# Kernel optimization log

Hardware: AMD Instinct MI355X
Metric: run time of the kernel (lower is better)

Reference implementation:

```python
import jax, jax.numpy as jnp
import numpy as np
from jax import lax

VOCAB = 32000
D_MODEL = 1024
N_LAYERS = 4
D_STATE = 8
D_CONV = 4
EXPAND = 2
D_INNER = EXPAND * D_MODEL          # 2048
DT_RANK = (D_MODEL + 15) // 16      # 64
B, L = 2, 1024


def setup_inputs() -> dict:
    key = jax.random.key(0)
    ks = jax.random.split(key, 20)
    s = 0.02
    inp = {
        "input_ids": jax.random.randint(ks[0], (B, L), 0, VOCAB, dtype=jnp.int32),
        "embed": jax.random.normal(ks[1], (VOCAB, D_MODEL), jnp.float32) * s,
        "in_proj_w": jax.random.normal(ks[2], (N_LAYERS, 2 * D_INNER, D_MODEL), jnp.float32) * s,
        "conv_w": jax.random.normal(ks[3], (N_LAYERS, D_INNER, 1, D_CONV), jnp.float32) * s,
        "conv_b": jnp.zeros((N_LAYERS, D_INNER), jnp.float32),
        "x_proj_w": jax.random.normal(ks[4], (N_LAYERS, DT_RANK + 2 * D_STATE, D_INNER), jnp.float32) * s,
        "dt_proj_w": jax.random.normal(ks[5], (N_LAYERS, D_INNER, DT_RANK), jnp.float32) * s,
        "dt_proj_b": jax.random.normal(ks[6], (N_LAYERS, D_INNER), jnp.float32) * 0.1,
        "A_log": jnp.broadcast_to(jnp.log(jnp.arange(1, D_STATE + 1, dtype=jnp.float32)),
                                  (N_LAYERS, D_INNER, D_STATE)) + 0.0,
        "D": jnp.ones((N_LAYERS, D_INNER), jnp.float32),
        "out_proj_w": jax.random.normal(ks[7], (N_LAYERS, D_MODEL, D_INNER), jnp.float32) * s,
        "ln_g": jnp.ones((N_LAYERS, D_MODEL), jnp.float32),
        "ln_b": jnp.zeros((N_LAYERS, D_MODEL), jnp.float32),
        "fn_g": jnp.ones((D_MODEL,), jnp.float32),
        "fn_b": jnp.zeros((D_MODEL,), jnp.float32),
        "fc_w": jax.random.normal(ks[8], (VOCAB, D_MODEL), jnp.float32) * s,
        "fc_b": jnp.zeros((VOCAB,), jnp.float32),
    }
    return inp


def layer_norm(x, g, b, eps=1e-5):
    mu = jnp.mean(x, -1, keepdims=True)
    var = jnp.var(x, -1, keepdims=True)
    return (x - mu) * lax.rsqrt(var + eps) * g + b


def silu(x):
    return x * jax.nn.sigmoid(x)


def selective_scan(deltaA, deltaBu, C):
    # deltaA, deltaBu: (b,l,d,n); C: (b,l,n) -> y: (b,l,d)
    def step(h, inp):
        dA, dBu, c = inp
        h = dA * h + dBu                       # (b,d,n)
        y = jnp.einsum('bdn,bn->bd', h, c)
        return h, y
    h0 = jnp.zeros(deltaA.shape[:1] + deltaA.shape[2:], deltaA.dtype)
    _, ys = lax.scan(step, h0, (deltaA.transpose(1, 0, 2, 3),
                                deltaBu.transpose(1, 0, 2, 3),
                                C.transpose(1, 0, 2)))
    return ys.transpose(1, 0, 2)


def mamba_block(x, in_proj_w, conv_w, conv_b, x_proj_w, dt_proj_w, dt_proj_b, A_log, D, out_proj_w):
    # x: (b,l,d_model)
    xz = jnp.einsum('bld,ed->ble', x, in_proj_w)          # (b,l,2*di)
    xc, z = jnp.split(xz, 2, axis=-1)
    # causal depthwise conv1d, kernel D_CONV
    xc_ncl = xc.transpose(0, 2, 1)                         # (b,di,l)
    xc_ncl = lax.conv_general_dilated(
        xc_ncl, conv_w, window_strides=(1,), padding=[(D_CONV - 1, 0)],
        feature_group_count=D_INNER, dimension_numbers=('NCH', 'OIH', 'NCH'))
    xc = silu(xc_ncl.transpose(0, 2, 1) + conv_b)          # (b,l,di)
    x_dbl = jnp.einsum('bld,ed->ble', xc, x_proj_w)        # (b,l,dt_rank+2n)
    dt, Bm, Cm = jnp.split(x_dbl, [DT_RANK, DT_RANK + D_STATE], axis=-1)
    dt = jax.nn.softplus(jnp.einsum('blr,dr->bld', dt, dt_proj_w) + dt_proj_b)  # (b,l,di)
    A = -jnp.exp(A_log)                                    # (di,n)
    deltaA = jnp.exp(dt[..., None] * A)                    # (b,l,di,n)
    deltaBu = dt[..., None] * Bm[:, :, None, :] * xc[..., None]
    y = selective_scan(deltaA, deltaBu, Cm)                # (b,l,di)
    y = y + xc * D
    y = y * silu(z)
    return jnp.einsum('ble,de->bld', y, out_proj_w)


def reference(input_ids, embed, in_proj_w, conv_w, conv_b, x_proj_w, dt_proj_w,
              dt_proj_b, A_log, D, out_proj_w, ln_g, ln_b, fn_g, fn_b, fc_w, fc_b):
    x = embed[input_ids]                                   # (b,l,d)
    for i in range(N_LAYERS):
        out = mamba_block(x, in_proj_w[i], conv_w[i], conv_b[i], x_proj_w[i],
                          dt_proj_w[i], dt_proj_b[i], A_log[i], D[i], out_proj_w[i])
        x = layer_norm(out + x, ln_g[i], ln_b[i])
    x = layer_norm(x, fn_g, fn_b)
    logits = jnp.einsum('bld,vd->blv', x, fc_w) + fc_b
    return logits
```

## Files before the change

kernel.cpp:

```cpp
#include <hip/hip_runtime.h>
#include <cstddef>
#include <cstdint>

#define D_MODEL 1024
#define D_INNER 2048
#define DT_RANK 64
#define D_STATE 8
#define NLAYERS 4
#define BATCH 2
#define SEQ 1024
#define M_ROWS (BATCH*SEQ)
#define VOCAB 32000
#define XPAD 128
#define NC 32
#define LC 32
#define XSK 8

typedef __attribute__((ext_vector_type(8))) short short8;
typedef __attribute__((ext_vector_type(4))) float f32x4;

#define GPTR(p) (const __attribute__((address_space(1))) void*)(p)
#define LPTR(p) (__attribute__((address_space(3))) void*)(p)

__device__ __forceinline__ float sigmoidf_(float x) { return 1.f / (1.f + __expf(-x)); }

__device__ __forceinline__ unsigned short f2bf(float f) {
    unsigned u = __float_as_uint(f);
    u += 0x7fffu + ((u >> 16) & 1u);
    return (unsigned short)(u >> 16);
}
__device__ __forceinline__ float bf2f(unsigned short u) {
    return __uint_as_float((unsigned)u << 16);
}

__global__ __launch_bounds__(256) void cast_kernel(const float* __restrict__ in,
                                                   unsigned short* __restrict__ out, int n4)
{
    int i = blockIdx.x * 256 + threadIdx.x;
    if (i >= n4) return;
    float4 v = ((const float4*)in)[i];
    ushort4 o;
    o.x = f2bf(v.x); o.y = f2bf(v.y); o.z = f2bf(v.z); o.w = f2bf(v.w);
    ((ushort4*)out)[i] = o;
}

__global__ __launch_bounds__(256) void cast_pad_xproj(const float* __restrict__ in,
                                                      unsigned short* __restrict__ out)
{
    int i = blockIdx.x * 256 + threadIdx.x;
    if (i >= NLAYERS * XPAD * D_INNER / 4) return;
    int col4 = i & (D_INNER / 4 - 1);
    int row = (i >> 9) & (XPAD - 1);
    int layer = i >> 16;
    ushort4 o = {0, 0, 0, 0};
    if (row < 80) {
        float4 v = ((const float4*)(in + ((size_t)layer * 80 + row) * D_INNER))[col4];
        o.x = f2bf(v.x); o.y = f2bf(v.y); o.z = f2bf(v.z); o.w = f2bf(v.w);
    }
    ((ushort4*)out)[i] = o;
}

__global__ __launch_bounds__(256) void gather_kernel(const int* __restrict__ ids,
                                                     const float* __restrict__ embed,
                                                     float* __restrict__ x,
                                                     unsigned short* __restrict__ xb)
{
    int m = blockIdx.x;
    int t = threadIdx.x;
    int id = ids[m];
    float4 v = ((const float4*)(embed + (size_t)id * D_MODEL))[t];
    ((float4*)(x + (size_t)m * D_MODEL))[t] = v;
    ushort4 o;
    o.x = f2bf(v.x); o.y = f2bf(v.y); o.z = f2bf(v.z); o.w = f2bf(v.w);
    ((ushort4*)(xb + (size_t)m * D_MODEL))[t] = o;
}

template<int EPI>
__global__ __launch_bounds__(256) void gemm_bf16_nt(const unsigned short* __restrict__ A, int lda,
                                                    const unsigned short* __restrict__ B, int ldb,
                                                    void* __restrict__ Cv, int ldc,
                                                    int K, const float* __restrict__ bias)
{
    __shared__ unsigned short As[2][128 * 32];
    __shared__ unsigned short Bs[2][128 * 32];
    const int tid = threadIdx.x;

    const int gm = gridDim.x;
    const int bid = blockIdx.y * gm + blockIdx.x;
    const int q = (gm * gridDim.y) >> 3;
    const int swz = (bid & 7) * q + (bid >> 3);
    const int bm = (swz % gm) * 128, bn = (swz / gm) * 128;

    const int wid = tid >> 6, lane = tid & 63;
    const int wm = (wid >> 1) * 64, wn = (wid & 1) * 64;
    const int lrow = lane & 15, lkg = lane >> 4;

    const int srow = tid >> 2;
    const int ksrc = ((tid & 3) ^ ((srow >> 1) & 3)) * 8;
    const size_t kz = (size_t)blockIdx.z * K;
    const unsigned short* Ag = A + (size_t)(bm + srow) * lda + kz + ksrc;
    const unsigned short* Bg = B + (size_t)(bn + srow) * ldb + kz + ksrc;
    const size_t r64a = (size_t)64 * lda;
    const size_t r64b = (size_t)64 * ldb;

#define STAGE(buf, koff)                                                                              \
    do {                                                                                              \
        __builtin_amdgcn_global_load_lds(GPTR(Ag + (koff)),        LPTR(&As[buf][tid * 8]), 16, 0, 0);\
        __builtin_amdgcn_global_load_lds(GPTR(Ag + r64a + (koff)), LPTR(&As[buf][2048 + tid * 8]), 16, 0, 0);\
        __builtin_amdgcn_global_load_lds(GPTR(Bg + (koff)),        LPTR(&Bs[buf][tid * 8]), 16, 0, 0);\
        __builtin_amdgcn_global_load_lds(GPTR(Bg + r64b + (koff)), LPTR(&Bs[buf][2048 + tid * 8]), 16, 0, 0);\
    } while (0)

    f32x4 acc[4][4];
    #pragma unroll
    for (int i = 0; i < 4; ++i)
        #pragma unroll
        for (int j = 0; j < 4; ++j)
            acc[i][j] = f32x4{0.f, 0.f, 0.f, 0.f};

    STAGE(0, 0);

    int cur = 0;
    for (int k0 = 0; k0 < K; k0 += 32) {
        if (k0 + 32 < K) {
            STAGE(cur ^ 1, k0 + 32);
            asm volatile("s_waitcnt vmcnt(4)" ::: "memory");
        } else {
            asm volatile("s_waitcnt vmcnt(0)" ::: "memory");
        }
        __builtin_amdgcn_s_barrier();
        __builtin_amdgcn_sched_barrier(0);

        short8 af[4], bf[4];
        #pragma unroll
        for (int i = 0; i < 4; ++i) {
            int ra = wm + 16 * i + lrow;
            int pa = lkg ^ ((ra >> 1) & 3);
            af[i] = *(const short8*)(&As[cur][ra * 32 + pa * 8]);
            int rb = wn + 16 * i + lrow;
            int pb = lkg ^ ((rb >> 1) & 3);
            bf[i] = *(const short8*)(&Bs[cur][rb * 32 + pb * 8]);
        }
        __builtin_amdgcn_s_setprio(1);
        #pragma unroll
        for (int i = 0; i < 4; ++i)
            #pragma unroll
            for (int j = 0; j < 4; ++j)
                acc[i][j] = __builtin_amdgcn_mfma_f32_16x16x32_bf16(af[i], bf[j], acc[i][j], 0, 0, 0);
        __builtin_amdgcn_s_setprio(0);

        __builtin_amdgcn_s_barrier();
        cur ^= 1;
    }
#undef STAGE

    const int crow = bm + wm + lkg * 4;
    const int ccol = bn + wn + lrow;
    #pragma unroll
    for (int i = 0; i < 4; ++i) {
        #pragma unroll
        for (int j = 0; j < 4; ++j) {
            float bv = (EPI == 2 || EPI == 3) ? bias[ccol + 16 * j] : 0.f;
            #pragma unroll
            for (int r = 0; r < 4; ++r) {
                float v = acc[i][j][r] + bv;
                size_t off = (size_t)(crow + 16 * i + r) * ldc + ccol + 16 * j;
                if (EPI == 0) {
                    ((float*)Cv)[(size_t)blockIdx.z * M_ROWS * ldc + off] = v;
                } else if (EPI == 2) {
                    ((float*)Cv)[off] = v;
                } else {
                    if (EPI == 3) v = (v > 20.f) ? v : log1pf(__expf(v));
                    ((unsigned short*)Cv)[off] = f2bf(v);
                }
            }
        }
    }
}

__device__ __forceinline__ void rd_a8(const unsigned short* S, int base, int lrow, int lkg, short8 a[4][2]) {
    #pragma unroll
    for (int i = 0; i < 4; ++i)
        #pragma unroll
        for (int kk = 0; kk < 2; ++kk) {
            int row = base + i * 16 + lrow;
            int p = (kk * 4 + lkg) ^ (lrow & 7);
            a[i][kk] = *(const short8*)(S + row * 64 + p * 8);
        }
}
__device__ __forceinline__ void rd_b4(const unsigned short* S, int base, int lrow, int lkg, short8 b[2][2]) {
    #pragma unroll
    for (int j = 0; j < 2; ++j)
        #pragma unroll
        for (int kk = 0; kk < 2; ++kk) {
            int row = base + j * 16 + lrow;
            int p = (kk * 4 + lkg) ^ (lrow & 7);
            b[j][kk] = *(const short8*)(S + row * 64 + p * 8);
        }
}

__global__ __launch_bounds__(512) void gemm_bf16_8ph(const unsigned short* __restrict__ A, int lda,
                                                     const unsigned short* __restrict__ B, int ldb,
                                                     float* __restrict__ C, int ldc,
                                                     int K, const float* __restrict__ bias)
{
    __shared__ unsigned short As[2][256 * 64];
    __shared__ unsigned short Bs[2][256 * 64];
    const int tid = threadIdx.x;

    const int gm = gridDim.x;
    const int bid = blockIdx.y * gm + blockIdx.x;
    const int q = (gm * gridDim.y) >> 3;
    const int swz = (bid & 7) * q + (bid >> 3);
    const int bm = (swz % gm) * 256, bn = (swz / gm) * 256;

    const int wid = tid >> 6, lane = tid & 63;
    const int wr = wid >> 2, wc = wid & 3;
    const int arow0 = wr * 128, brow0 = wc * 64;
    const int lrow = lane & 15, lkg = lane >> 4;

    const int sg = tid >> 3, su = tid & 7;
    const int ksrc = (su ^ (sg & 7)) * 8;
    const unsigned short* Ag = A + (size_t)(bm + sg) * lda + ksrc;
    const unsigned short* Bg = B + (size_t)(bn + sg) * ldb + ksrc;

#define STG_A(buf, kt) do {                                                                                        \
    __builtin_amdgcn_global_load_lds(GPTR(Ag + (size_t)(kt) * 64),                       LPTR(&As[buf][tid * 8]), 16, 0, 0); \
    __builtin_amdgcn_global_load_lds(GPTR(Ag + (size_t)(kt) * 64 + (size_t)64 * lda),    LPTR(&As[buf][4096 + tid * 8]), 16, 0, 0); \
    __builtin_amdgcn_global_load_lds(GPTR(Ag + (size_t)(kt) * 64 + (size_t)128 * lda),   LPTR(&As[buf][8192 + tid * 8]), 16, 0, 0); \
    __builtin_amdgcn_global_load_lds(GPTR(Ag + (size_t)(kt) * 64 + (size_t)192 * lda),   LPTR(&As[buf][12288 + tid * 8]), 16, 0, 0); \
} while (0)
#define STG_B(buf, kt) do {                                                                                        \
    __builtin_amdgcn_global_load_lds(GPTR(Bg + (size_t)(kt) * 64),                       LPTR(&Bs[buf][tid * 8]), 16, 0, 0); \
    __builtin_amdgcn_global_load_lds(GPTR(Bg + (size_t)(kt) * 64 + (size_t)64 * ldb),    LPTR(&Bs[buf][4096 + tid * 8]), 16, 0, 0); \
    __builtin_amdgcn_global_load_lds(GPTR(Bg + (size_t)(kt) * 64 + (size_t)128 * ldb),   LPTR(&Bs[buf][8192 + tid * 8]), 16, 0, 0); \
    __builtin_amdgcn_global_load_lds(GPTR(Bg + (size_t)(kt) * 64 + (size_t)192 * ldb),   LPTR(&Bs[buf][12288 + tid * 8]), 16, 0, 0); \
} while (0)
#define MFMA_Q(IH, JH) do {                                                                                        \
    __builtin_amdgcn_s_setprio(1);                                                                                 \
    _Pragma("unroll") for (int i = 0; i < 4; ++i)                                                                  \
    _Pragma("unroll") for (int j = 0; j < 2; ++j)                                                                  \
    _Pragma("unroll") for (int kk = 0; kk < 2; ++kk)                                                               \
        acc[(IH) * 4 + i][(JH) * 2 + j] =                                                                          \
            __builtin_amdgcn_mfma_f32_16x16x32_bf16(a[i][kk], b[j][kk], acc[(IH) * 4 + i][(JH) * 2 + j], 0, 0, 0); \
    __builtin_amdgcn_s_setprio(0);                                                                                 \
} while (0)
#define PBAR() __builtin_amdgcn_s_barrier()

    f32x4 acc[8][4];
    #pragma unroll
    for (int i = 0; i < 8; ++i)
        #pragma unroll
        for (int j = 0; j < 4; ++j)
            acc[i][j] = f32x4{0.f, 0.f, 0.f, 0.f};

    short8 a[4][2], b[2][2];
    const int NT = K >> 6;

    STG_A(0, 0); STG_B(0, 0); STG_A(1, 1);
    asm volatile("s_waitcnt vmcnt(4)" ::: "memory");
    PBAR();

    int buf = 0;
    for (int U = 0; U < NT; ++U, buf ^= 1) {
        if (U + 1 < NT) STG_B(buf ^ 1, U + 1);
        rd_a8(As[buf], arow0, lrow, lkg, a);
        rd_b4(Bs[buf], brow0, lrow, lkg, b);
        PBAR(); __builtin_amdgcn_sched_barrier(0);
        MFMA_Q(0, 0);
        PBAR();
        rd_b4(Bs[buf], brow0 + 32, lrow, lkg, b);
        PBAR(); __builtin_amdgcn_sched_barrier(0);
        MFMA_Q(0, 1);
        PBAR();
        rd_a8(As[buf], arow0 + 64, lrow, lkg, a);
        PBAR(); __builtin_amdgcn_sched_barrier(0);
        MFMA_Q(1, 1);
        PBAR();
        rd_b4(Bs[buf], brow0, lrow, lkg, b);
        if (U + 2 < NT) {
            STG_A(buf, U + 2);
            asm volatile("s_waitcnt vmcnt(4)" ::: "memory");
        } else {
            asm volatile("s_waitcnt vmcnt(0)" ::: "memory");
        }
        PBAR(); __builtin_amdgcn_sched_barrier(0);
        MFMA_Q(1, 0);
        PBAR();
    }
#undef STG_A
#undef STG_B
#undef MFMA_Q
#undef PBAR

    const int crow = bm + arow0 + lkg * 4;
    const int ccol = bn + brow0 + lrow;
    #pragma unroll
    for (int i = 0; i < 8; ++i) {
        #pragma unroll
        for (int j = 0; j < 4; ++j) {
            float bv = bias[ccol + 16 * j];
            float* Cp = C + (size_t)(crow + 16 * i) * ldc + ccol + 16 * j;
            #pragma unroll
            for (int r = 0; r < 4; ++r)
                Cp[(size_t)r * ldc] = acc[i][j][r] + bv;
        }
    }
}

__global__ __launch_bounds__(256) void reduce_xdbl(const float* __restrict__ part,
                                                   float* __restrict__ xdbl,
                                                   unsigned short* __restrict__ xdbl_b)
{
    int i = blockIdx.x * 256 + threadIdx.x;
    float4 s = ((const float4*)part)[i];
    #pragma unroll
    for (int z = 1; z < XSK; ++z) {
        float4 v = ((const float4*)part)[(size_t)z * (M_ROWS * XPAD / 4) + i];
        s.x += v.x; s.y += v.y; s.z += v.z; s.w += v.w;
    }
    ((float4*)xdbl)[i] = s;
    ushort4 o;
    o.x = f2bf(s.x); o.y = f2bf(s.y); o.z = f2bf(s.z); o.w = f2bf(s.w);
    ((ushort4*)xdbl_b)[i] = o;
}

__global__ __launch_bounds__(256) void conv_silu_kernel(const unsigned short* __restrict__ xzb,
                                                        const float* __restrict__ cw,
                                                        const float* __restrict__ cb,
                                                        unsigned short* __restrict__ xcb)
{
    int idx = blockIdx.x * 256 + threadIdx.x;
    int d = idx & (D_INNER - 1);
    int m = idx >> 11;
    int l = m & (SEQ - 1);
    int b = m >> 10;
    float w0 = cw[d * 4 + 0], w1 = cw[d * 4 + 1], w2 = cw[d * 4 + 2], w3 = cw[d * 4 + 3];
    float s = cb[d];
    const unsigned short* base = xzb + ((size_t)b * SEQ) * (2 * D_INNER) + d;
    if (l - 3 >= 0) s += bf2f(base[(size_t)(l - 3) * (2 * D_INNER)]) * w0;
    if (l - 2 >= 0) s += bf2f(base[(size_t)(l - 2) * (2 * D_INNER)]) * w1;
    if (l - 1 >= 0) s += bf2f(base[(size_t)(l - 1) * (2 * D_INNER)]) * w2;
    s += bf2f(base[(size_t)l * (2 * D_INNER)]) * w3;
    float v = s * sigmoidf_(s);
    xcb[(size_t)m * D_INNER + d] = f2bf(v);
}

__global__ __launch_bounds__(256) void scan_partial(const unsigned short* __restrict__ dtb,
                                                    const float* __restrict__ xdbl,
                                                    const unsigned short* __restrict__ xcb,
                                                    const float* __restrict__ A_log,
                                                    float* __restrict__ H,
                                                    float* __restrict__ P)
{
    const int tid = threadIdx.x;
    const int b = blockIdx.x & 1;
    const int c = (blockIdx.x >> 1) & (NC - 1);
    const int d = ((blockIdx.x >> 6) << 8) + tid;

    __shared__ float Bsm[LC][8];
    {
        int r = tid >> 3, n = tid & 7;
        Bsm[r][n] = xdbl[(size_t)(b * SEQ + c * LC + r) * XPAD + DT_RANK + n];
    }
    __syncthreads();

    float An[8];
    #pragma unroll
    for (int n = 0; n < 8; ++n) An[n] = -__expf(A_log[d * 8 + n]);
    float h[8] = {0.f,0.f,0.f,0.f,0.f,0.f,0.f,0.f};
    float p[8] = {1.f,1.f,1.f,1.f,1.f,1.f,1.f,1.f};

    const unsigned short* dtp = dtb + (size_t)(b * SEQ + c * LC) * D_INNER + d;
    const unsigned short* xcp = xcb + (size_t)(b * SEQ + c * LC) * D_INNER + d;
    for (int l = 0; l < LC; ++l) {
        float dtv = bf2f(dtp[(size_t)l * D_INNER]);
        float ux  = dtv * bf2f(xcp[(size_t)l * D_INNER]);
        #pragma unroll
        for (int n = 0; n < 8; ++n) {
            float dA = __expf(dtv * An[n]);
            h[n] = dA * h[n] + Bsm[l][n] * ux;
            p[n] *= dA;
        }
    }
    size_t base = (size_t)((b * NC + c) * 8) * D_INNER + d;
    #pragma unroll
    for (int n = 0; n < 8; ++n) {
        H[base + (size_t)n * D_INNER] = h[n];
        P[base + (size_t)n * D_INNER] = p[n];
    }
}

__global__ __launch_bounds__(256) void scan_combine(const float* __restrict__ H,
                                                    float* __restrict__ P )
{
    int idx = blockIdx.x * 256 + threadIdx.x;
    int d = idx & (D_INNER - 1);
    int n = (idx >> 11) & 7;
    int b = idx >> 14;
    float hp = 0.f;
    for (int c = 0; c < NC; ++c) {
        size_t base = (size_t)((b * NC + c) * 8 + n) * D_INNER + d;
        float Pv = P[base], Hv = H[base];
        P[base] = hp;
        hp = Pv * hp + Hv;
    }
}

__global__ __launch_bounds__(256) void scan_final(const unsigned short* __restrict__ dtb,
                                                  const float* __restrict__ xdbl,
                                                  const unsigned short* __restrict__ xcb,
                                                  const unsigned short* __restrict__ xzb,
                                                  const float* __restrict__ A_log,
                                                  const float* __restrict__ Dp,
                                                  const float* __restrict__ h0,
                                                  unsigned short* __restrict__ yb)
{
    const int tid = threadIdx.x;
    const int b = blockIdx.x & 1;
    const int c = (blockIdx.x >> 1) & (NC - 1);
    const int d = ((blockIdx.x >> 6) << 8) + tid;

    __shared__ float Bsm[LC][8];
    __shared__ float Csm[LC][8];
    {
        int r = tid >> 3, n = tid & 7;
        size_t xrow = (size_t)(b * SEQ + c * LC + r) * XPAD;
        Bsm[r][n] = xdbl[xrow + DT_RANK + n];
        Csm[r][n] = xdbl[xrow + DT_RANK + 8 + n];
    }
    __syncthreads();

    float An[8], h[8];
    size_t base = (size_t)((b * NC + c) * 8) * D_INNER + d;
    #pragma unroll
    for (int n = 0; n < 8; ++n) {
        An[n] = -__expf(A_log[d * 8 + n]);
        h[n] = h0[base + (size_t)n * D_INNER];
    }
    const float Dv = Dp[d];

    const unsigned short* dtp = dtb + (size_t)(b * SEQ + c * LC) * D_INNER + d;
    const unsigned short* xcp = xcb + (size_t)(b * SEQ + c * LC) * D_INNER + d;
    const unsigned short* zp  = xzb + (size_t)(b * SEQ + c * LC) * (2 * D_INNER) + D_INNER + d;
    unsigned short* ybp = yb + (size_t)(b * SEQ + c * LC) * D_INNER + d;

    for (int l = 0; l < LC; ++l) {
        float dtv = bf2f(dtp[(size_t)l * D_INNER]);
        float xcv = bf2f(xcp[(size_t)l * D_INNER]);
        float zv  = bf2f(zp[(size_t)l * (2 * D_INNER)]);
        float ux = dtv * xcv;
        float acc = 0.f;
        #pragma unroll
        for (int n = 0; n < 8; ++n) {
            float dA = __expf(dtv * An[n]);
            h[n] = dA * h[n] + Bsm[l][n] * ux;
            acc += h[n] * Csm[l][n];
        }
        float yv = (acc + xcv * Dv) * (zv * sigmoidf_(zv));
        ybp[(size_t)l * D_INNER] = f2bf(yv);
    }
}

template<bool ADD>
__global__ __launch_bounds__(256) void ln_kernel(const float* __restrict__ extra,
                                                 const float* __restrict__ xin,
                                                 float* __restrict__ xout,
                                                 unsigned short* __restrict__ xbout,
                                                 const float* __restrict__ g,
                                                 const float* __restrict__ bb)
{
    int m = blockIdx.x;
    int t = threadIdx.x;
    float4 v = ((const float4*)(xin + (size_t)m * D_MODEL))[t];
    if (ADD) {
        float4 e = ((const float4*)(extra + (size_t)m * D_MODEL))[t];
        v.x += e.x; v.y += e.y; v.z += e.z; v.w += e.w;
    }
    float s  = v.x + v.y + v.z + v.w;
    float s2 = v.x * v.x + v.y * v.y + v.z * v.z + v.w * v.w;
    for (int off = 32; off; off >>= 1) {
        s  += __shfl_down(s, off);
        s2 += __shfl_down(s2, off);
    }
    __shared__ float red[8];
    int wid = t >> 6, lane = t & 63;
    if (lane == 0) { red[wid] = s; red[wid + 4] = s2; }
    __syncthreads();
    if (t == 0) {
        float a  = red[0] + red[1] + red[2] + red[3];
        float b2 = red[4] + red[5] + red[6] + red[7];
        float mu = a * (1.f / D_MODEL);
        red[0] = mu;
        red[4] = b2 * (1.f / D_MODEL) - mu * mu;
    }
    __syncthreads();
    float mu = red[0];
    float rs = rsqrtf(red[4] + 1e-5f);
    float4 gg = ((const float4*)g)[t];
    float4 bv = ((const float4*)bb)[t];
    float4 o;
    o.x = (v.x - mu) * rs * gg.x + bv.x;
    o.y = (v.y - mu) * rs * gg.y + bv.y;
    o.z = (v.z - mu) * rs * gg.z + bv.z;
    o.w = (v.w - mu) * rs * gg.w + bv.w;
    ((float4*)(xout + (size_t)m * D_MODEL))[t] = o;
    ushort4 ob;
    ob.x = f2bf(o.x); ob.y = f2bf(o.y); ob.z = f2bf(o.z); ob.w = f2bf(o.w);
    ((ushort4*)(xbout + (size_t)m * D_MODEL))[t] = ob;
}

extern "C" void kernel_launch(void* const* d_in, const int* in_sizes, int n_in,
                              void* d_out, int out_size, void* d_ws, size_t ws_size,
                              hipStream_t stream)
{
    const int*   ids      = (const int*)d_in[0];
    const float* embed    = (const float*)d_in[1];
    const float* in_proj  = (const float*)d_in[2];
    const float* conv_w   = (const float*)d_in[3];
    const float* conv_b   = (const float*)d_in[4];
    const float* x_proj   = (const float*)d_in[5];
    const float* dt_w     = (const float*)d_in[6];
    const float* dt_b     = (const float*)d_in[7];
    const float* A_log    = (const float*)d_in[8];
    const float* Dp       = (const float*)d_in[9];
    const float* out_proj = (const float*)d_in[10];
    const float* ln_g     = (const float*)d_in[11];
    const float* ln_b     = (const float*)d_in[12];
    const float* fn_g     = (const float*)d_in[13];
    const float* fn_b     = (const float*)d_in[14];
    const float* fc_w     = (const float*)d_in[15];
    const float* fc_b     = (const float*)d_in[16];
    float* logits = (float*)d_out;

    float* ws = (float*)d_ws;
    float* x     = ws;
    float* xdbl  = x + (size_t)M_ROWS * D_MODEL;
    float* tmp   = xdbl + (size_t)M_ROWS * XPAD;
    float* xpart = tmp + (size_t)M_ROWS * D_MODEL;

    float* Hbuf = tmp;
    float* Pbuf = tmp + (size_t)BATCH * NC * D_STATE * D_INNER;

    unsigned short* xb     = (unsigned short*)(xpart + (size_t)XSK * M_ROWS * XPAD);
    unsigned short* yb     = xb + (size_t)M_ROWS * D_MODEL;
    unsigned short* xzb    = yb + (size_t)M_ROWS * D_INNER;
    unsigned short* xcb    = xzb + (size_t)M_ROWS * 2 * D_INNER;
    unsigned short* dtb    = xcb + (size_t)M_ROWS * D_INNER;
    unsigned short* xdbl_b = dtb + (size_t)M_ROWS * D_INNER;
    unsigned short* wb_in  = xdbl_b + (size_t)M_ROWS * XPAD;
    unsigned short* wb_out = wb_in + (size_t)NLAYERS * 2 * D_INNER * D_MODEL;
    unsigned short* wb_fc  = wb_out + (size_t)NLAYERS * D_MODEL * D_INNER;
    unsigned short* wb_x   = wb_fc + (size_t)VOCAB * D_MODEL;
    unsigned short* wb_dt  = wb_x + (size_t)NLAYERS * XPAD * D_INNER;

    {
        int n4 = NLAYERS * 2 * D_INNER * D_MODEL / 4;
        cast_kernel<<<(n4 + 255) / 256, 256, 0, stream>>>(in_proj, wb_in, n4);
        n4 = NLAYERS * D_MODEL * D_INNER / 4;
        cast_kernel<<<(n4 + 255) / 256, 256, 0, stream>>>(out_proj, wb_out, n4);
        n4 = VOCAB * D_MODEL / 4;
        cast_kernel<<<(n4 + 255) / 256, 256, 0, stream>>>(fc_w, wb_fc, n4);
        n4 = NLAYERS * D_INNER * DT_RANK / 4;
        cast_kernel<<<(n4 + 255) / 256, 256, 0, stream>>>(dt_w, wb_dt, n4);
        n4 = NLAYERS * XPAD * D_INNER / 4;
        cast_pad_xproj<<<(n4 + 255) / 256, 256, 0, stream>>>(x_proj, wb_x);
    }

    gather_kernel<<<M_ROWS, 256, 0, stream>>>(ids, embed, x, xb);

    for (int i = 0; i < NLAYERS; ++i) {
        const unsigned short* W_in_b  = wb_in + (size_t)i * 2 * D_INNER * D_MODEL;
        const unsigned short* W_out_b = wb_out + (size_t)i * D_MODEL * D_INNER;
        const unsigned short* W_x_b   = wb_x + (size_t)i * XPAD * D_INNER;
        const unsigned short* W_dt_b  = wb_dt + (size_t)i * D_INNER * DT_RANK;
        const float* cw    = conv_w + (size_t)i * D_INNER * 4;
        const float* cb    = conv_b + (size_t)i * D_INNER;
        const float* b_dt  = dt_b + (size_t)i * D_INNER;
        const float* Al    = A_log + (size_t)i * D_INNER * D_STATE;
        const float* Dl    = Dp + (size_t)i * D_INNER;
        const float* g     = ln_g + (size_t)i * D_MODEL;
        const float* bb    = ln_b + (size_t)i * D_MODEL;

        gemm_bf16_nt<1><<<dim3(M_ROWS / 128, 2 * D_INNER / 128), 256, 0, stream>>>(
            xb, D_MODEL, W_in_b, D_MODEL, xzb, 2 * D_INNER, D_MODEL, nullptr);

        conv_silu_kernel<<<(M_ROWS * D_INNER) / 256, 256, 0, stream>>>(xzb, cw, cb, xcb);

        gemm_bf16_nt<0><<<dim3(M_ROWS / 128, 1, XSK), 256, 0, stream>>>(
            xcb, D_INNER, W_x_b, D_INNER, xpart, XPAD, D_INNER / XSK, nullptr);
        reduce_xdbl<<<(M_ROWS * XPAD / 4) / 256, 256, 0, stream>>>(xpart, xdbl, xdbl_b);

        gemm_bf16_nt<3><<<dim3(M_ROWS / 128, D_INNER / 128), 256, 0, stream>>>(
            xdbl_b, XPAD, W_dt_b, DT_RANK, dtb, D_INNER, DT_RANK, b_dt);

        scan_partial<<<BATCH * NC * (D_INNER / 256), 256, 0, stream>>>(
            dtb, xdbl, xcb, Al, Hbuf, Pbuf);
        scan_combine<<<(BATCH * D_STATE * D_INNER) / 256, 256, 0, stream>>>(Hbuf, Pbuf);
        scan_final<<<BATCH * NC * (D_INNER / 256), 256, 0, stream>>>(
            dtb, xdbl, xcb, xzb, Al, Dl, Pbuf, yb);

        gemm_bf16_nt<0><<<dim3(M_ROWS / 128, D_MODEL / 128), 256, 0, stream>>>(
            yb, D_INNER, W_out_b, D_INNER, tmp, D_MODEL, D_INNER, nullptr);

        ln_kernel<true><<<M_ROWS, 256, 0, stream>>>(tmp, x, x, xb, g, bb);
    }

    ln_kernel<false><<<M_ROWS, 256, 0, stream>>>(nullptr, x, tmp, xb, fn_g, fn_b);

    gemm_bf16_8ph<<<dim3(M_ROWS / 256, VOCAB / 256), 512, 0, stream>>>(
        xb, D_MODEL, wb_fc, D_MODEL, logits, VOCAB, D_MODEL, fc_b);
}
```

Baseline: 1.002 ms.

## Split-K out_proj and x_proj, and pipeline LM-head GEMM loads per half-tile

The LM-head 8-phase GEMM now stages A and B in half-tile chunks spread across the phases of a two-tile unrolled loop. Each warp also takes two separated 32-column B slices instead of one contiguous 64-column slice. This is meant to smooth memory traffic against MFMA work and shorten exposed load waits. Separately, out_proj becomes split-K by 2, with the partial sums added inside the residual LayerNorm, and x_proj split-K goes from 8 to 16 to raise parallelism in small GEMMs. The cost is more partial-buffer traffic and more complex wait counting.

```diff
diff --git a/kernel.cpp b/kernel.cpp
--- a/kernel.cpp
+++ b/kernel.cpp
@@ -14,7 +14,8 @@
 #define XPAD 128
 #define NC 32
 #define LC 32
-#define XSK 8
+#define XSK 16
+#define OSK 2
 
 typedef __attribute__((ext_vector_type(8))) short short8;
 typedef __attribute__((ext_vector_type(4))) float f32x4;
@@ -216,7 +217,8 @@
 
     const int wid = tid >> 6, lane = tid & 63;
     const int wr = wid >> 2, wc = wid & 3;
-    const int arow0 = wr * 128, brow0 = wc * 64;
+    const int arow0 = wr * 128;
+    const int b0r = wc * 32, b1r = 128 + wc * 32;
     const int lrow = lane & 15, lkg = lane >> 4;
 
     const int sg = tid >> 3, su = tid & 7;
@@ -224,28 +226,32 @@
     const unsigned short* Ag = A + (size_t)(bm + sg) * lda + ksrc;
     const unsigned short* Bg = B + (size_t)(bn + sg) * ldb + ksrc;
 
-#define STG_A(buf, kt) do {                                                                                        \
-    __builtin_amdgcn_global_load_lds(GPTR(Ag + (size_t)(kt) * 64),                       LPTR(&As[buf][tid * 8]), 16, 0, 0); \
-    __builtin_amdgcn_global_load_lds(GPTR(Ag + (size_t)(kt) * 64 + (size_t)64 * lda),    LPTR(&As[buf][4096 + tid * 8]), 16, 0, 0); \
-    __builtin_amdgcn_global_load_lds(GPTR(Ag + (size_t)(kt) * 64 + (size_t)128 * lda),   LPTR(&As[buf][8192 + tid * 8]), 16, 0, 0); \
-    __builtin_amdgcn_global_load_lds(GPTR(Ag + (size_t)(kt) * 64 + (size_t)192 * lda),   LPTR(&As[buf][12288 + tid * 8]), 16, 0, 0); \
+#define STG_A_H(buf, kt, h) do {                                                                   \
+    __builtin_amdgcn_global_load_lds(GPTR(Ag + (size_t)(kt) * 64 + (size_t)((h) * 128) * lda),     \
+                                     LPTR(&As[buf][(h) * 8192 + tid * 8]), 16, 0, 0);              \
+    __builtin_amdgcn_global_load_lds(GPTR(Ag + (size_t)(kt) * 64 + (size_t)((h) * 128 + 64) * lda),\
+                                     LPTR(&As[buf][(h) * 8192 + 4096 + tid * 8]), 16, 0, 0);       \
 } while (0)
-#define STG_B(buf, kt) do {                                                                                        \
-    __builtin_amdgcn_global_load_lds(GPTR(Bg + (size_t)(kt) * 64),                       LPTR(&Bs[buf][tid * 8]), 16, 0, 0); \
-    __builtin_amdgcn_global_load_lds(GPTR(Bg + (size_t)(kt) * 64 + (size_t)64 * ldb),    LPTR(&Bs[buf][4096 + tid * 8]), 16, 0, 0); \
-    __builtin_amdgcn_global_load_lds(GPTR(Bg + (size_t)(kt) * 64 + (size_t)128 * ldb),   LPTR(&Bs[buf][8192 + tid * 8]), 16, 0, 0); \
-    __builtin_amdgcn_global_load_lds(GPTR(Bg + (size_t)(kt) * 64 + (size_t)192 * ldb),   LPTR(&Bs[buf][12288 + tid * 8]), 16, 0, 0); \
+#define STG_B_H(buf, kt, h) do {                                                                   \
+    __builtin_amdgcn_global_load_lds(GPTR(Bg + (size_t)(kt) * 64 + (size_t)((h) * 128) * ldb),     \
+                                     LPTR(&Bs[buf][(h) * 8192 + tid * 8]), 16, 0, 0);              \
+    __builtin_amdgcn_global_load_lds(GPTR(Bg + (size_t)(kt) * 64 + (size_t)((h) * 128 + 64) * ldb),\
+                                     LPTR(&Bs[buf][(h) * 8192 + 4096 + tid * 8]), 16, 0, 0);       \
 } while (0)
-#define MFMA_Q(IH, JH) do {                                                                                        \
-    __builtin_amdgcn_s_setprio(1);                                                                                 \
-    _Pragma("unroll") for (int i = 0; i < 4; ++i)                                                                  \
-    _Pragma("unroll") for (int j = 0; j < 2; ++j)                                                                  \
-    _Pragma("unroll") for (int kk = 0; kk < 2; ++kk)                                                               \
-        acc[(IH) * 4 + i][(JH) * 2 + j] =                                                                          \
-            __builtin_amdgcn_mfma_f32_16x16x32_bf16(a[i][kk], b[j][kk], acc[(IH) * 4 + i][(JH) * 2 + j], 0, 0, 0); \
-    __builtin_amdgcn_s_setprio(0);                                                                                 \
+#define WAIT4() asm volatile("s_waitcnt vmcnt(4)" ::: "memory")
+#define WAIT0() asm volatile("s_waitcnt vmcnt(0)" ::: "memory")
+#define PBAR() __builtin_amdgcn_s_barrier()
+#define SBAR() __builtin_amdgcn_sched_barrier(0)
+#define MFMA_Q(QA, BH) do {                                                                        \
+    __builtin_amdgcn_s_setprio(1);                                                                 \
+    _Pragma("unroll") for (int i = 0; i < 4; ++i)                                                  \
+    _Pragma("unroll") for (int j = 0; j < 2; ++j)                                                  \
+    _Pragma("unroll") for (int kk = 0; kk < 2; ++kk)                                               \
+        acc[(QA) * 4 + i][(BH) * 2 + j] =                                                          \
+            __builtin_amdgcn_mfma_f32_16x16x32_bf16(a[i][kk], b[j][kk],                            \
+                                                    acc[(QA) * 4 + i][(BH) * 2 + j], 0, 0, 0);     \
+    __builtin_amdgcn_s_setprio(0);                                                                 \
 } while (0)
-#define PBAR() __builtin_amdgcn_s_barrier()
 
     f32x4 acc[8][4];
     #pragma unroll
@@ -256,51 +262,76 @@
 
     short8 a[4][2], b[2][2];
     const int NT = K >> 6;
-
-    STG_A(0, 0); STG_B(0, 0); STG_A(1, 1);
-    asm volatile("s_waitcnt vmcnt(4)" ::: "memory");
+    const int NI = NT >> 1;
+
+    STG_A_H(0, 0, 0); STG_A_H(0, 0, 1); STG_B_H(0, 0, 0); STG_B_H(0, 0, 1);
+    STG_A_H(1, 1, 0);
+    asm volatile("s_waitcnt vmcnt(2)" ::: "memory");
     PBAR();
 
-    int buf = 0;
-    for (int U = 0; U < NT; ++U, buf ^= 1) {
-        if (U + 1 < NT) STG_B(buf ^ 1, U + 1);
-        rd_a8(As[buf], arow0, lrow, lkg, a);
-        rd_b4(Bs[buf], brow0, lrow, lkg, b);
-        PBAR(); __builtin_amdgcn_sched_barrier(0);
+    for (int it = 0; it < NI; ++it) {
+        const int T0 = 2 * it, T1 = 2 * it + 1;
+        const bool more = (it + 1 < NI);
+
+        STG_A_H(1, T1, 1);
+        rd_a8(As[0], arow0, lrow, lkg, a);
+        rd_b4(Bs[0], b0r, lrow, lkg, b);
+        WAIT4(); PBAR(); SBAR();
         MFMA_Q(0, 0);
         PBAR();
-        rd_b4(Bs[buf], brow0 + 32, lrow, lkg, b);
-        PBAR(); __builtin_amdgcn_sched_barrier(0);
+        STG_B_H(1, T1, 0);
+        rd_b4(Bs[0], b1r, lrow, lkg, b);
+        WAIT4(); PBAR(); SBAR();
         MFMA_Q(0, 1);
         PBAR();
-        rd_a8(As[buf], arow0 + 64, lrow, lkg, a);
-        PBAR(); __builtin_amdgcn_sched_barrier(0);
+        STG_B_H(1, T1, 1);
+        rd_a8(As[0], arow0 + 64, lrow, lkg, a);
+        WAIT4(); PBAR(); SBAR();
         MFMA_Q(1, 1);
         PBAR();
-        rd_b4(Bs[buf], brow0, lrow, lkg, b);
-        if (U + 2 < NT) {
-            STG_A(buf, U + 2);
-            asm volatile("s_waitcnt vmcnt(4)" ::: "memory");
-        } else {
-            asm volatile("s_waitcnt vmcnt(0)" ::: "memory");
-        }
-        PBAR(); __builtin_amdgcn_sched_barrier(0);
+        rd_b4(Bs[0], b0r, lrow, lkg, b);
+        if (more) { STG_A_H(0, T0 + 2, 0); WAIT4(); } else { WAIT0(); }
+        PBAR(); SBAR();
         MFMA_Q(1, 0);
         PBAR();
-    }
-#undef STG_A
-#undef STG_B
+        if (more) STG_A_H(0, T0 + 2, 1);
+        rd_a8(As[1], arow0, lrow, lkg, a);
+        rd_b4(Bs[1], b0r, lrow, lkg, b);
+        WAIT4(); PBAR(); SBAR();
+        MFMA_Q(0, 0);
+        PBAR();
+        if (more) STG_B_H(0, T0 + 2, 0);
+        rd_b4(Bs[1], b1r, lrow, lkg, b);
+        WAIT4(); PBAR(); SBAR();
+        MFMA_Q(0, 1);
+        PBAR();
+        if (more) STG_B_H(0, T0 + 2, 1);
+        rd_a8(As[1], arow0 + 64, lrow, lkg, a);
+        WAIT4(); PBAR(); SBAR();
+        MFMA_Q(1, 1);
+        PBAR();
+        rd_b4(Bs[1], b0r, lrow, lkg, b);
+        if (more) { STG_A_H(1, T1 + 2, 0); WAIT4(); } else { WAIT0(); }
+        PBAR(); SBAR();
+        MFMA_Q(1, 0);
+        PBAR();
+    }
+#undef STG_A_H
+#undef STG_B_H
+#undef WAIT4
+#undef WAIT0
+#undef PBAR
+#undef SBAR
 #undef MFMA_Q
-#undef PBAR
 
     const int crow = bm + arow0 + lkg * 4;
-    const int ccol = bn + brow0 + lrow;
     #pragma unroll
     for (int i = 0; i < 8; ++i) {
         #pragma unroll
         for (int j = 0; j < 4; ++j) {
-            float bv = bias[ccol + 16 * j];
-            float* Cp = C + (size_t)(crow + 16 * i) * ldc + ccol + 16 * j;
+            int ccol = bn + (j >> 1) * 128 + wc * 32 + (j & 1) * 16 + lrow;
+            float bv = bias[ccol];
+            float* Cp = C + (size_t)(crow + 16 * i) * ldc + ccol;
             #pragma unroll
             for (int r = 0; r < 4; ++r)
                 Cp[(size_t)r * ldc] = acc[i][j][r] + bv;
@@ -462,8 +493,9 @@
     }
 }
 
-template<bool ADD>
-__global__ __launch_bounds__(256) void ln_kernel(const float* __restrict__ extra,
+template<int NEXTRA>
+__global__ __launch_bounds__(256) void ln_kernel(const float* __restrict__ e0,
+                                                 const float* __restrict__ e1,
                                                  const float* __restrict__ xin,
                                                  float* __restrict__ xout,
                                                  unsigned short* __restrict__ xbout,
@@ -473,8 +505,12 @@
     int m = blockIdx.x;
     int t = threadIdx.x;
     float4 v = ((const float4*)(xin + (size_t)m * D_MODEL))[t];
-    if (ADD) {
-        float4 e = ((const float4*)(extra + (size_t)m * D_MODEL))[t];
+    if (NEXTRA >= 1) {
+        float4 e = ((const float4*)(e0 + (size_t)m * D_MODEL))[t];
+        v.x += e.x; v.y += e.y; v.z += e.z; v.w += e.w;
+    }
+    if (NEXTRA >= 2) {
+        float4 e = ((const float4*)(e1 + (size_t)m * D_MODEL))[t];
         v.x += e.x; v.y += e.y; v.z += e.z; v.w += e.w;
     }
     float s  = v.x + v.y + v.z + v.w;
@@ -541,6 +577,7 @@
 
     float* Hbuf = tmp;
     float* Pbuf = tmp + (size_t)BATCH * NC * D_STATE * D_INNER;
+    float* opart = xpart;
 
     unsigned short* xb     = (unsigned short*)(xpart + (size_t)XSK * M_ROWS * XPAD);
     unsigned short* yb     = xb + (size_t)M_ROWS * D_MODEL;
@@ -600,13 +637,14 @@
         scan_final<<<BATCH * NC * (D_INNER / 256), 256, 0, stream>>>(
             dtb, xdbl, xcb, xzb, Al, Dl, Pbuf, yb);
 
-        gemm_bf16_nt<0><<<dim3(M_ROWS / 128, D_MODEL / 128), 256, 0, stream>>>(
-            yb, D_INNER, W_out_b, D_INNER, tmp, D_MODEL, D_INNER, nullptr);
-
-        ln_kernel<true><<<M_ROWS, 256, 0, stream>>>(tmp, x, x, xb, g, bb);
-    }
-
-    ln_kernel<false><<<M_ROWS, 256, 0, stream>>>(nullptr, x, tmp, xb, fn_g, fn_b);
+        gemm_bf16_nt<0><<<dim3(M_ROWS / 128, D_MODEL / 128, OSK), 256, 0, stream>>>(
+            yb, D_INNER, W_out_b, D_INNER, opart, D_MODEL, D_INNER / OSK, nullptr);
+
+        ln_kernel<2><<<M_ROWS, 256, 0, stream>>>(
+            opart, opart + (size_t)M_ROWS * D_MODEL, x, x, xb, g, bb);
+    }
+
+    ln_kernel<0><<<M_ROWS, 256, 0, stream>>>(nullptr, nullptr, x, tmp, xb, fn_g, fn_b);
 
     gemm_bf16_8ph<<<dim3(M_ROWS / 256, VOCAB / 256), 512, 0, stream>>>(
         xb, D_MODEL, wb_fc, D_MODEL, logits, VOCAB, D_MODEL, fc_b);
```

Result: faster. 899.1 us (-10.3%).
